# Kernel tuning notes

Hardware: AMD Instinct MI355X
Metric: run time of the kernel (lower is better)

Reference implementation:

```python
import jax, jax.numpy as jnp
import numpy as np

N_NODES = 100000
N_EDGES = 1600000
NFEAT = 256
NHID = 64
DROPOUT = 0.5


def setup_inputs() -> dict:
    key = jax.random.key(0)
    ks = jax.random.split(key, 6)
    x = jax.random.normal(ks[0], (N_NODES, NFEAT), dtype=jnp.float32)
    W = jax.random.normal(ks[1], (NFEAT, NHID), dtype=jnp.float32) * (1.0 / np.sqrt(NFEAT))
    b = jax.random.normal(ks[2], (NHID,), dtype=jnp.float32) * 0.01
    edge_src = jax.random.randint(ks[3], (N_EDGES,), 0, N_NODES, dtype=jnp.int32)
    edge_dst = jax.random.randint(ks[4], (N_EDGES,), 0, N_NODES, dtype=jnp.int32)
    edge_weight = jax.random.uniform(ks[5], (N_EDGES,), dtype=jnp.float32)
    return {"x": x, "W": W, "b": b, "edge_src": edge_src,
            "edge_dst": edge_dst, "edge_weight": edge_weight}


def reference(x, W, b, edge_src, edge_dst, edge_weight):
    n = x.shape[0]
    # GraphConvolution: support = x @ W ; out = spmm(adj, support) + b
    support = x @ W                                   # [N, nhid]
    msg = support[edge_src] * edge_weight[:, None]    # [E, nhid] gather + scale
    agg = jax.ops.segment_sum(msg, edge_dst, num_segments=n)  # scatter-add [N, nhid]
    h = jax.nn.relu(agg + b)
    # F.dropout(training=True): inverted dropout with keep prob 1-p
    keep = 1.0 - DROPOUT
    mask = jax.random.bernoulli(jax.random.key(42), keep, h.shape)
    return jnp.where(mask, h / keep, jnp.zeros_like(h))
```

## Files before the change

kernel.cpp:

```cpp
#include <hip/hip_runtime.h>
#include <stdint.h>

#define N_NODES 100000
#define N_EDGES 1600000
#define NFEAT 256
#define NHID 64
#define TILE 32
#define NBKT ((N_NODES + TILE - 1) / TILE)
#define NBIN 49
#define BINCAP 33600
#define BCAP 832
#define BUFCAP 832
#define EPB 2048
#define FILLB ((N_EDGES + EPB - 1) / EPB)
#define GEMMB ((N_NODES + 63) / 64)
#define K1_BLOCKS 2346
#define K2_CHUNKS 17
#define K2_BLOCKS (NBIN * K2_CHUNKS)

typedef __attribute__((ext_vector_type(8))) short sh8;
typedef __attribute__((ext_vector_type(4))) float f4;

__device__ __forceinline__ unsigned short f2bf(float f) {
  unsigned u = __float_as_uint(f);
  u = (u + 0x7FFFu + ((u >> 16) & 1u)) >> 16;
  return (unsigned short)u;
}

__global__ __launch_bounds__(256) void gcn_gemm_or_l1(
    const float* __restrict__ x, const float* __restrict__ W,
    unsigned short* __restrict__ support,
    const int* __restrict__ esrc, const int* __restrict__ edst,
    const float* __restrict__ ew,
    int* __restrict__ gcur, int2* __restrict__ lcell) {
  __shared__ short Wt[NHID][264];
  __shared__ int lhist[NBIN];
  __shared__ int lbaseg[NBIN];
  const int tid = threadIdx.x;
  const int b = blockIdx.x;

  if ((b % 3) != 2) {
    const int gb = (b / 3) * 2 + (b % 3);
    if (gb >= GEMMB) return;

    for (int i = tid; i < NFEAT * NHID; i += 256) {
      int k = i >> 6, c = i & 63;
      Wt[c][k] = (short)f2bf(W[i]);
    }
    __syncthreads();

    const int w = tid >> 6;
    const int l = tid & 63;
    const int r16 = l & 15;
    const int kg = l >> 4;

    const int row = gb * 64 + w * 16 + r16;
    const int rowc = row < N_NODES ? row : N_NODES - 1;
    const float* xr = x + (size_t)rowc * NFEAT;

    const f4 z = {0.f, 0.f, 0.f, 0.f};
    f4 acc0 = z, acc1 = z, acc2 = z, acc3 = z;

#pragma unroll
    for (int ks = 0; ks < 8; ++ks) {
      const int k0 = ks * 32 + kg * 8;
      float4 v0 = *reinterpret_cast<const float4*>(&xr[k0]);
      float4 v1 = *reinterpret_cast<const float4*>(&xr[k0 + 4]);
      sh8 a;
      a[0] = (short)f2bf(v0.x); a[1] = (short)f2bf(v0.y);
      a[2] = (short)f2bf(v0.z); a[3] = (short)f2bf(v0.w);
      a[4] = (short)f2bf(v1.x); a[5] = (short)f2bf(v1.y);
      a[6] = (short)f2bf(v1.z); a[7] = (short)f2bf(v1.w);

      sh8 b0 = *reinterpret_cast<const sh8*>(&Wt[r16][k0]);
      sh8 b1 = *reinterpret_cast<const sh8*>(&Wt[16 + r16][k0]);
      sh8 b2 = *reinterpret_cast<const sh8*>(&Wt[32 + r16][k0]);
      sh8 b3 = *reinterpret_cast<const sh8*>(&Wt[48 + r16][k0]);
      acc0 = __builtin_amdgcn_mfma_f32_16x16x32_bf16(a, b0, acc0, 0, 0, 0);
      acc1 = __builtin_amdgcn_mfma_f32_16x16x32_bf16(a, b1, acc1, 0, 0, 0);
      acc2 = __builtin_amdgcn_mfma_f32_16x16x32_bf16(a, b2, acc2, 0, 0, 0);
      acc3 = __builtin_amdgcn_mfma_f32_16x16x32_bf16(a, b3, acc3, 0, 0, 0);
    }

    const int orow_base = gb * 64 + w * 16 + kg * 4;
#pragma unroll
    for (int reg = 0; reg < 4; ++reg) {
      const int orow = orow_base + reg;
      if (orow < N_NODES) {
        unsigned short* sp = &support[(size_t)orow * NHID + r16];
        sp[0]  = f2bf(acc0[reg]);
        sp[16] = f2bf(acc1[reg]);
        sp[32] = f2bf(acc2[reg]);
        sp[48] = f2bf(acc3[reg]);
      }
    }
  } else {
    const int fb = b / 3;
    const int base = fb * EPB;
    if (tid < NBIN) lhist[tid] = 0;
    __syncthreads();

    int rx[8], bin[8], rank[8];
    float ry[8];
#pragma unroll
    for (int it = 0; it < 8; ++it) {
      int e = base + it * 256 + tid;
      if (e < N_EDGES) {
        int d = edst[e];
        rx[it] = esrc[e] | ((d & 2047) << 17);
        ry[it] = ew[e];
        bin[it] = d >> 11;
        rank[it] = atomicAdd(&lhist[bin[it]], 1);
      } else {
        bin[it] = -1;
      }
    }
    __syncthreads();
    if (tid < NBIN) {
      int c = lhist[tid];
      if (c > 0) lbaseg[tid] = atomicAdd(&gcur[tid], c);
    }
    __syncthreads();
#pragma unroll
    for (int it = 0; it < 8; ++it) {
      if (bin[it] >= 0) {
        lcell[(size_t)bin[it] * BINCAP + lbaseg[bin[it]] + rank[it]] =
            make_int2(rx[it], __float_as_int(ry[it]));
      }
    }
  }
}

__global__ __launch_bounds__(256) void gcn_l2part(const int* __restrict__ gcur,
                                                  const int2* __restrict__ lcell,
                                                  int* __restrict__ cnt,
                                                  unsigned* __restrict__ rec) {
  __shared__ int lhist[64];
  __shared__ int gbase[64];
  const int tid = threadIdx.x;
  const int bin = blockIdx.x / K2_CHUNKS;
  const int ck = blockIdx.x % K2_CHUNKS;
  const int nbin = gcur[bin];
  const int start = ck * 2048;
  const int m = nbin - start;
  if (m <= 0) return;

  if (tid < 64) lhist[tid] = 0;
  __syncthreads();

  unsigned r4[8];
  int lb[8], rank[8];
#pragma unroll
  for (int it = 0; it < 8; ++it) {
    int j = it * 256 + tid;
    if (j < m && j < 2048) {
      int2 rc = lcell[(size_t)bin * BINCAP + start + j];
      unsigned ux = (unsigned)rc.x;
      int d = bin * 2048 + (int)(ux >> 17);
      float w = __int_as_float(rc.y);
      int q = (int)(w * 1024.0f);
      q = q > 1023 ? 1023 : q;
      lb[it] = (d >> 5) - bin * 64;
      r4[it] = (ux & 0x1FFFFu) | ((unsigned)(d & 31) << 17) | ((unsigned)q << 22);
      rank[it] = atomicAdd(&lhist[lb[it]], 1);
    } else {
      lb[it] = -1;
    }
  }
  __syncthreads();
  if (tid < 64) {
    int gb = bin * 64 + tid;
    int c = lhist[tid];
    if (gb < NBKT && c > 0) gbase[tid] = atomicAdd(&cnt[gb], c);
  }
  __syncthreads();
#pragma unroll
  for (int it = 0; it < 8; ++it) {
    if (lb[it] >= 0) {
      int bucket = bin * 64 + lb[it];
      rec[(size_t)bucket * BCAP + gbase[lb[it]] + rank[it]] = r4[it];
    }
  }
}

__device__ __forceinline__ unsigned rotl32(unsigned x, int r) {
  return (x << r) | (x >> (32 - r));
}

__device__ __forceinline__ unsigned threefry_bits(unsigned i) {
  const unsigned ks0 = 0u, ks1 = 42u;
  const unsigned ks2 = 0x1BD11BDAu ^ ks0 ^ ks1;
  unsigned x0 = ks0;
  unsigned x1 = i + ks1;
#define TF_R4(a, bb, c, d)                       \
  x0 += x1; x1 = rotl32(x1, a);  x1 ^= x0;       \
  x0 += x1; x1 = rotl32(x1, bb); x1 ^= x0;       \
  x0 += x1; x1 = rotl32(x1, c);  x1 ^= x0;       \
  x0 += x1; x1 = rotl32(x1, d);  x1 ^= x0;
  TF_R4(13, 15, 26, 6);  x0 += ks1; x1 += ks2 + 1u;
  TF_R4(17, 29, 16, 24); x0 += ks2; x1 += ks0 + 2u;
  TF_R4(13, 15, 26, 6);  x0 += ks0; x1 += ks1 + 3u;
  TF_R4(17, 29, 16, 24); x0 += ks1; x1 += ks2 + 4u;
  TF_R4(13, 15, 26, 6);  x0 += ks2; x1 += ks0 + 5u;
#undef TF_R4
  return x0 ^ x1;
}

__global__ __launch_bounds__(256) void gcn_pull_fused(const unsigned* __restrict__ support2,
                                                      const int* __restrict__ cnt,
                                                      const unsigned* __restrict__ rec,
                                                      const float* __restrict__ bias,
                                                      float* __restrict__ out) {
  __shared__ int cntl[TILE];
  __shared__ int base[TILE];
  __shared__ int cur[TILE];
  __shared__ unsigned buf[BUFCAP];

  const int t = threadIdx.x;
  const int b = blockIdx.x;
  const int n = cnt[b];
  const unsigned* cell = &rec[(size_t)b * BCAP];

  if (t < TILE) cntl[t] = 0;
  __syncthreads();

  for (int j = t; j < n; j += 256)
    atomicAdd(&cntl[(cell[j] >> 17) & (TILE - 1)], 1);
  __syncthreads();
  if (t == 0) {
    int run = 0;
#pragma unroll
    for (int i = 0; i < TILE; ++i) {
      base[i] = run;
      run += cntl[i];
    }
  }
  __syncthreads();
  if (t < TILE) cur[t] = base[t];
  __syncthreads();

  for (int j = t; j < n; j += 256) {
    unsigned r = cell[j];
    int slot = atomicAdd(&cur[(r >> 17) & (TILE - 1)], 1);
    buf[slot] = r;
  }
  __syncthreads();

  const int hw = t >> 5;
  const int l = t & 31;
  const int f = l * 2;
  const float2 bb = *reinterpret_cast<const float2*>(&bias[f]);
  const float qs = 1.0f / 1024.0f;

#pragma unroll
  for (int ns = 0; ns < 4; ++ns) {
    const int nl = hw + ns * 8;
    const int node = b * TILE + nl;
    int j = base[nl];
    const int end = j + cntl[nl];
    float acc0 = 0.f, acc1 = 0.f;
    for (; j + 1 < end; j += 2) {
      unsigned r0 = buf[j];
      unsigned r1 = buf[j + 1];
      unsigned p0 = support2[(size_t)(r0 & 0x1FFFF) * 32 + l];
      unsigned p1 = support2[(size_t)(r1 & 0x1FFFF) * 32 + l];
      float w0 = ((float)(r0 >> 22) + 0.5f) * qs;
      float w1 = ((float)(r1 >> 22) + 0.5f) * qs;
      acc0 = fmaf(__uint_as_float(p0 << 16), w0, acc0);
      acc1 = fmaf(__uint_as_float(p0 & 0xFFFF0000u), w0, acc1);
      acc0 = fmaf(__uint_as_float(p1 << 16), w1, acc0);
      acc1 = fmaf(__uint_as_float(p1 & 0xFFFF0000u), w1, acc1);
    }
    if (j < end) {
      unsigned r0 = buf[j];
      unsigned p0 = support2[(size_t)(r0 & 0x1FFFF) * 32 + l];
      float w0 = ((float)(r0 >> 22) + 0.5f) * qs;
      acc0 = fmaf(__uint_as_float(p0 << 16), w0, acc0);
      acc1 = fmaf(__uint_as_float(p0 & 0xFFFF0000u), w0, acc1);
    }

    float h0 = fmaxf(acc0 + bb.x, 0.f) * 2.0f;
    float h1 = fmaxf(acc1 + bb.y, 0.f) * 2.0f;
    unsigned i0 = (unsigned)node * 64u + (unsigned)f;
    unsigned m0 = threefry_bits(i0);
    unsigned m1 = threefry_bits(i0 + 1u);
    float2 o;
    o.x = (m0 & 0x80000000u) ? 0.f : h0;
    o.y = (m1 & 0x80000000u) ? 0.f : h1;
    *reinterpret_cast<float2*>(&out[i0]) = o;
  }
}

extern "C" void kernel_launch(void* const* d_in, const int* in_sizes, int n_in,
                              void* d_out, int out_size, void* d_ws, size_t ws_size,
                              hipStream_t stream) {
  const float* x = (const float*)d_in[0];
  const float* W = (const float*)d_in[1];
  const float* b = (const float*)d_in[2];
  const int* esrc = (const int*)d_in[3];
  const int* edst = (const int*)d_in[4];
  const float* ew = (const float*)d_in[5];
  float* out = (float*)d_out;

  char* ws = (char*)d_ws;
  unsigned short* support = (unsigned short*)ws;
  int* cnt   = (int*)(ws + 12800000);
  int* gcur  = (int*)(ws + 12812500);
  unsigned* rec = (unsigned*)(ws + 12812800);
  int2* lcell = (int2*)(ws + 23212800);

  hipMemsetAsync(cnt, 0, 12756, stream);

  gcn_gemm_or_l1<<<K1_BLOCKS, 256, 0, stream>>>(x, W, support, esrc, edst, ew,
                                                gcur, lcell);
  gcn_l2part<<<K2_BLOCKS, 256, 0, stream>>>(gcur, lcell, cnt, rec);
  gcn_pull_fused<<<NBKT, 256, 0, stream>>>((const unsigned*)support, cnt, rec, b, out);
}
```

Measured before the change: 104.5 us.

## Rebalance GEMM/fill block interleave, prepack W fragments, use packed bf16 convert

Changes the fused kernel's block split from 2 GEMM blocks per fill block to a 1:1 interleave. Each GEMM block now computes two 64-row tiles, so the per-block W staging into LDS is amortized over twice the work. W is stored in LDS pre-arranged in MFMA fragment order, giving conflict-free vector reads. Activations and W are converted with the hardware packed bf16 instruction instead of manual rounding. The trade-off is fewer, longer GEMM blocks and a shared LDS buffer aliased for the histogram arrays.

```diff
diff --git a/kernel.cpp b/kernel.cpp
--- a/kernel.cpp
+++ b/kernel.cpp
@@ -14,7 +14,7 @@
 #define EPB 2048
 #define FILLB ((N_EDGES + EPB - 1) / EPB)
 #define GEMMB ((N_NODES + 63) / 64)
-#define K1_BLOCKS 2346
+#define K1_BLOCKS (FILLB * 2)
 #define K2_CHUNKS 17
 #define K2_BLOCKS (NBIN * K2_CHUNKS)
 
@@ -26,6 +26,14 @@
   u = (u + 0x7FFFu + ((u >> 16) & 1u)) >> 16;
   return (unsigned short)u;
 }
+
+__device__ __forceinline__ unsigned cvt_pk_bf16(float lo, float hi) {
+  unsigned r;
+  asm("v_cvt_pk_bf16_f32 %0, %1, %2" : "=v"(r) : "v"(lo), "v"(hi));
+  return r;
+}
+
+union FragU { sh8 v; unsigned u[4]; };
 
 __global__ __launch_bounds__(256) void gcn_gemm_or_l1(
     const float* __restrict__ x, const float* __restrict__ W,
@@ -33,19 +41,26 @@
     const int* __restrict__ esrc, const int* __restrict__ edst,
     const float* __restrict__ ew,
     int* __restrict__ gcur, int2* __restrict__ lcell) {
-  __shared__ short Wt[NHID][264];
-  __shared__ int lhist[NBIN];
-  __shared__ int lbaseg[NBIN];
+  __shared__ sh8 Wf[2048];
   const int tid = threadIdx.x;
   const int b = blockIdx.x;
 
-  if ((b % 3) != 2) {
-    const int gb = (b / 3) * 2 + (b % 3);
-    if (gb >= GEMMB) return;
-
-    for (int i = tid; i < NFEAT * NHID; i += 256) {
-      int k = i >> 6, c = i & 63;
-      Wt[c][k] = (short)f2bf(W[i]);
+  if ((b & 1) == 0) {
+    const int gb = b >> 1;
+
+#pragma unroll
+    for (int i = 0; i < 8; ++i) {
+      int f = i * 256 + tid;
+      int col = ((f >> 4) & 3) * 16 + (f & 15);
+      int k0 = (f >> 8) * 32 + ((f >> 6) & 3) * 8;
+      FragU uu;
+#pragma unroll
+      for (int j = 0; j < 4; ++j) {
+        float lo = W[(k0 + 2 * j) * NHID + col];
+        float hi = W[(k0 + 2 * j + 1) * NHID + col];
+        uu.u[j] = cvt_pk_bf16(lo, hi);
+      }
+      Wf[f] = uu.v;
     }
     __syncthreads();
 
@@ -54,48 +69,55 @@
     const int r16 = l & 15;
     const int kg = l >> 4;
 
-    const int row = gb * 64 + w * 16 + r16;
-    const int rowc = row < N_NODES ? row : N_NODES - 1;
-    const float* xr = x + (size_t)rowc * NFEAT;
-
-    const f4 z = {0.f, 0.f, 0.f, 0.f};
-    f4 acc0 = z, acc1 = z, acc2 = z, acc3 = z;
-
-#pragma unroll
-    for (int ks = 0; ks < 8; ++ks) {
-      const int k0 = ks * 32 + kg * 8;
-      float4 v0 = *reinterpret_cast<const float4*>(&xr[k0]);
-      float4 v1 = *reinterpret_cast<const float4*>(&xr[k0 + 4]);
-      sh8 a;
-      a[0] = (short)f2bf(v0.x); a[1] = (short)f2bf(v0.y);
-      a[2] = (short)f2bf(v0.z); a[3] = (short)f2bf(v0.w);
-      a[4] = (short)f2bf(v1.x); a[5] = (short)f2bf(v1.y);
-      a[6] = (short)f2bf(v1.z); a[7] = (short)f2bf(v1.w);
-
-      sh8 b0 = *reinterpret_cast<const sh8*>(&Wt[r16][k0]);
-      sh8 b1 = *reinterpret_cast<const sh8*>(&Wt[16 + r16][k0]);
-      sh8 b2 = *reinterpret_cast<const sh8*>(&Wt[32 + r16][k0]);
-      sh8 b3 = *reinterpret_cast<const sh8*>(&Wt[48 + r16][k0]);
-      acc0 = __builtin_amdgcn_mfma_f32_16x16x32_bf16(a, b0, acc0, 0, 0, 0);
-      acc1 = __builtin_amdgcn_mfma_f32_16x16x32_bf16(a, b1, acc1, 0, 0, 0);
-      acc2 = __builtin_amdgcn_mfma_f32_16x16x32_bf16(a, b2, acc2, 0, 0, 0);
-      acc3 = __builtin_amdgcn_mfma_f32_16x16x32_bf16(a, b3, acc3, 0, 0, 0);
-    }
-
-    const int orow_base = gb * 64 + w * 16 + kg * 4;
-#pragma unroll
-    for (int reg = 0; reg < 4; ++reg) {
-      const int orow = orow_base + reg;
-      if (orow < N_NODES) {
-        unsigned short* sp = &support[(size_t)orow * NHID + r16];
-        sp[0]  = f2bf(acc0[reg]);
-        sp[16] = f2bf(acc1[reg]);
-        sp[32] = f2bf(acc2[reg]);
-        sp[48] = f2bf(acc3[reg]);
+    for (int tt = 0; tt < 2; ++tt) {
+      const int gt = gb + tt * FILLB;
+      if (gt >= GEMMB) break;
+      const int row = gt * 64 + w * 16 + r16;
+      const int rowc = row < N_NODES ? row : N_NODES - 1;
+      const float* xr = x + (size_t)rowc * NFEAT;
+
+      const f4 z = {0.f, 0.f, 0.f, 0.f};
+      f4 acc0 = z, acc1 = z, acc2 = z, acc3 = z;
+
+#pragma unroll
+      for (int ks = 0; ks < 8; ++ks) {
+        const int k0 = ks * 32 + kg * 8;
+        float4 v0 = *reinterpret_cast<const float4*>(&xr[k0]);
+        float4 v1 = *reinterpret_cast<const float4*>(&xr[k0 + 4]);
+        FragU au;
+        au.u[0] = cvt_pk_bf16(v0.x, v0.y);
+        au.u[1] = cvt_pk_bf16(v0.z, v0.w);
+        au.u[2] = cvt_pk_bf16(v1.x, v1.y);
+        au.u[3] = cvt_pk_bf16(v1.z, v1.w);
+
+        const int fb_ = ks * 256 + kg * 64 + r16;
+        sh8 b0 = Wf[fb_];
+        sh8 b1 = Wf[fb_ + 16];
+        sh8 b2 = Wf[fb_ + 32];
+        sh8 b3 = Wf[fb_ + 48];
+        acc0 = __builtin_amdgcn_mfma_f32_16x16x32_bf16(au.v, b0, acc0, 0, 0, 0);
+        acc1 = __builtin_amdgcn_mfma_f32_16x16x32_bf16(au.v, b1, acc1, 0, 0, 0);
+        acc2 = __builtin_amdgcn_mfma_f32_16x16x32_bf16(au.v, b2, acc2, 0, 0, 0);
+        acc3 = __builtin_amdgcn_mfma_f32_16x16x32_bf16(au.v, b3, acc3, 0, 0, 0);
+      }
+
+      const int orow_base = gt * 64 + w * 16 + kg * 4;
+#pragma unroll
+      for (int reg = 0; reg < 4; ++reg) {
+        const int orow = orow_base + reg;
+        if (orow < N_NODES) {
+          unsigned short* sp = &support[(size_t)orow * NHID + r16];
+          sp[0]  = f2bf(acc0[reg]);
+          sp[16] = f2bf(acc1[reg]);
+          sp[32] = f2bf(acc2[reg]);
+          sp[48] = f2bf(acc3[reg]);
+        }
       }
     }
   } else {
-    const int fb = b / 3;
+    int* lhist = (int*)Wf;
+    int* lbaseg = ((int*)Wf) + 64;
+    const int fb = b >> 1;
     const int base = fb * EPB;
     if (tid < NBIN) lhist[tid] = 0;
     __syncthreads();
```

Measured after the change: 104.8 us. About the same (+0.3%).
